# Performance work log

Measured on AMD Instinct MI355X. Metric: run time of the kernel, lower is better.

## Reference

```python
import jax, jax.numpy as jnp
import numpy as np

B, N, D = 64, 256, 768
ITER_STEPS = 1


def _linear_w(key, out_d, in_d):
    s = 1.0 / np.sqrt(in_d)
    return jax.random.uniform(key, (out_d, in_d), jnp.float32, -s, s)


def setup_inputs() -> dict:
    key = jax.random.key(0)
    ks = jax.random.split(key, 16)
    node = jax.random.normal(ks[0], (B, N, D), jnp.float32)
    node_mask = jnp.ones((B, N), jnp.int32)
    argument_graph = jax.random.randint(ks[1], (B, N, N), 0, 2, jnp.int32)
    punctuation_graph = jax.random.randint(ks[2], (B, N, N), 0, 2, jnp.int32)
    inp = {
        "node": node,
        "node_mask": node_mask,
        "argument_graph": argument_graph,
        "punctuation_graph": punctuation_graph,
        # node-relatedness scorer: Linear(D, 1, bias=True)
        "Wq": _linear_w(ks[3], 1, D),
        "bq": jnp.zeros((1,), jnp.float32),
        # self node fc: Linear(D, D, bias=True)
        "Ws": _linear_w(ks[4], D, D),
        "bs": jnp.zeros((D,), jnp.float32),
        # 8 relation projections, Linear(D, D, bias=False)
        "Wa": _linear_w(ks[5], D, D),
        "Wp": _linear_w(ks[6], D, D),
        "Wap": _linear_w(ks[7], D, D),
        "Wpp": _linear_w(ks[8], D, D),
        "Wa2": _linear_w(ks[9], D, D),
        "Wp2": _linear_w(ks[10], D, D),
        "Wap2": _linear_w(ks[11], D, D),
        "Wpp2": _linear_w(ks[12], D, D),
    }
    return inp


def reference(node, node_mask, argument_graph, punctuation_graph,
              Wq, bq, Ws, bs, Wa, Wp, Wap, Wpp, Wa2, Wp2, Wap2, Wpp2):
    f32 = jnp.float32
    mask = node_mask.astype(f32)                      # [B, N]
    n = node.shape[1]
    eye = jnp.eye(n, dtype=f32)
    # dd_graph: node_mask outer product with zeroed diagonal
    dd = mask[:, None, :] * mask[:, :, None] * (1.0 - eye)   # [B, N, N]
    g_a = dd * argument_graph.astype(f32)
    g_p = dd * punctuation_graph.astype(f32)
    # reverse directed edges
    g_ar = dd * jnp.swapaxes(g_a, 1, 2)
    g_pr = dd * jnp.swapaxes(g_p, 1, 2)
    neigh = g_a.sum(-1) + g_p.sum(-1) + g_ar.sum(-1) + g_pr.sum(-1)  # [B, N]
    denom = jnp.where(neigh >= 1.0, neigh, 1.0)

    all_weight = []
    for _ in range(ITER_STEPS):
        # (1) node relatedness
        dw = jax.nn.sigmoid(jnp.einsum('bnd,od->bno', node, Wq) + bq)[..., 0]  # [B, N]
        all_weight.append(dw)
        self_info = jnp.einsum('bnd,ed->bne', node, Ws) + bs

        def msg(g, W):
            # node_weight: broadcast dw over rows, zero where no edge
            nw = dw[:, None, :] * g                    # [B, N, N]
            proj = jnp.einsum('bnd,ed->bne', node, W)  # [B, N, D]
            return jnp.matmul(nw, proj)                # [B, N, D]

        agg = (msg(g_a, Wa) + msg(g_p, Wp) + msg(g_ar, Wap) + msg(g_pr, Wpp)
               + msg(g_a, Wa2) + msg(g_p, Wp2) + msg(g_ar, Wap2) + msg(g_pr, Wpp2))
        agg = agg / denom[..., None]
        # (3) node update
        node = jax.nn.relu(self_info + agg)

    all_weight = jnp.stack(all_weight, axis=1)  # [B, steps, N]
    return node, all_weight
```

## Files before the change

### kernel.cpp

```cpp
#include <hip/hip_runtime.h>
#include <hip/hip_bf16.h>
#include <math.h>

typedef __bf16 bf16;
typedef unsigned char u8;
typedef unsigned long long ull;
typedef __bf16 bf16x8 __attribute__((ext_vector_type(8)));
typedef float f32x4 __attribute__((ext_vector_type(4)));

#define BB 64
#define NN 256
#define DD 768
#define MM (BB*NN)
#define KP 1024
#define WSZ (DD*DD)
#define TL2 272
#define AROW2 196608


__device__ __forceinline__ void async16(const void* g, void* l) {
  __builtin_amdgcn_global_load_lds((__attribute__((address_space(1))) void*)g,
                                   (__attribute__((address_space(3))) void*)l,
                                   16, 0, 0);
}

__device__ __forceinline__ void mma_step_fp8t(const char* lA, const char* lB,
                                              f32x4 acc[4][4], int lane, int wr, int wc) {
  long af[4], bfr[4];
  int koq = (lane >> 4) * 1024;
  int mA = (wr * 64 + (lane & 15)) * 8;
  int mB = (wc * 64 + (lane & 15)) * 8;
#pragma unroll
  for (int r = 0; r < 4; ++r)
    af[r] = *(const long*)(lA + koq + mA + r * 128);
#pragma unroll
  for (int c = 0; c < 4; ++c)
    bfr[c] = *(const long*)(lB + koq + mB + c * 128);
#pragma unroll
  for (int r = 0; r < 4; ++r)
#pragma unroll
    for (int c = 0; c < 4; ++c)
      acc[r][c] = __builtin_amdgcn_mfma_f32_16x16x32_fp8_fp8(af[r], bfr[c], acc[r][c], 0, 0, 0);
}

__device__ __forceinline__ void mma_step_sw(const char* lA, const char* lB,
                                            f32x4 acc[4][4], int lane, int wr, int wc) {
  bf16x8 af[4], bfr[4];
  int rbase = wr * 64 + (lane & 15);
  int cbase = wc * 64 + (lane & 15);
  int sSw = ((lane >> 4) ^ (((lane & 15) >> 1) & 3)) * 16;
#pragma unroll
  for (int r = 0; r < 4; ++r)
    af[r] = *(const bf16x8*)(lA + (rbase + r * 16) * 64 + sSw);
#pragma unroll
  for (int c = 0; c < 4; ++c)
    bfr[c] = *(const bf16x8*)(lB + (cbase + c * 16) * 64 + sSw);
#pragma unroll
  for (int r = 0; r < 4; ++r)
#pragma unroll
    for (int c = 0; c < 4; ++c)
      acc[r][c] = __builtin_amdgcn_mfma_f32_16x16x32_bf16(af[r], bfr[c], acc[r][c], 0, 0, 0);
}

__device__ __forceinline__ unsigned pack4(float a, float b, float c, float d) {
  int w = 0;
  w = __builtin_amdgcn_cvt_pk_fp8_f32(a, b, w, false);
  w = __builtin_amdgcn_cvt_pk_fp8_f32(c, d, w, true);
  return (unsigned)w;
}

__global__ void k_pre(const float* __restrict__ node, const float* __restrict__ Wq,
                      const float* __restrict__ bq, bf16* __restrict__ node_bf,
                      float* __restrict__ dw, float* __restrict__ allw,
                      float* __restrict__ neigh,
                      const float* __restrict__ Ws,
                      const float* __restrict__ Wa, const float* __restrict__ Wp,
                      const float* __restrict__ Wap, const float* __restrict__ Wpp,
                      const float* __restrict__ Wa2, const float* __restrict__ Wp2,
                      const float* __restrict__ Wap2, const float* __restrict__ Wpp2,
                      bf16* __restrict__ Wcat4, bf16* __restrict__ Ws_bf) {
  if (blockIdx.x < MM / 4) {
    int lane = threadIdx.x & 63, wv = threadIdx.x >> 6;
    int row = blockIdx.x * 4 + wv;
    const float* nr = node + (size_t)row * DD;
    bf16* nb = node_bf + (size_t)row * DD;
    float s = 0.f;
#pragma unroll
    for (int k = 0; k < DD / 64; ++k) {
      int idx = lane + k * 64;
      float v = nr[idx];
      nb[idx] = (bf16)v;
      s += v * Wq[idx];
    }
#pragma unroll
    for (int off = 32; off; off >>= 1) s += __shfl_down(s, off);
    if (lane == 0) {
      float z = s + bq[0];
      float d = 1.f / (1.f + expf(-z));
      dw[row] = d;
      allw[row] = d;
      neigh[row] = 0.f;
    }
  } else {
    int i = (blockIdx.x - MM / 4) * 256 + threadIdx.x;
    Ws_bf[i] = (bf16)Ws[i];
    Wcat4[i]           = (bf16)(Wa[i] + Wa2[i]);
    Wcat4[i + WSZ]     = (bf16)(Wp[i] + Wp2[i]);
    Wcat4[i + 2 * WSZ] = (bf16)(Wap[i] + Wap2[i]);
    Wcat4[i + 3 * WSZ] = (bf16)(Wpp[i] + Wpp2[i]);
  }
}

__device__ __forceinline__ void store_tiled(u8* base, int tile, int kin, int m, uint4 v) {
  size_t o = (size_t)tile * 4096 + (size_t)((kin >> 3) * 1024 + m * 8);
  *(ull*)(base + o)        = ((ull)v.y << 32) | v.x;
  *(ull*)(base + o + 1024) = ((ull)v.w << 32) | v.z;
}

__global__ void k_graph(const int* __restrict__ mask, const int* __restrict__ arg,
                        const int* __restrict__ pun, const float* __restrict__ dw,
                        u8* __restrict__ g8, float* __restrict__ neigh) {
  __shared__ float la[64][65];
  __shared__ float lp[64][65];
  __shared__ float msk[256];
  __shared__ float dwv[256];
  int tid = threadIdx.x;
  int bi = blockIdx.x;
  int b = bi >> 4, it = (bi >> 2) & 3, jt = bi & 3;
  int i0 = it * 64, j0 = jt * 64;
  msk[tid] = (float)mask[b * NN + tid];
  dwv[tid] = dw[b * NN + tid];
  __syncthreads();
  int ir = tid >> 2, c4 = (tid & 3) * 16;
  int i = i0 + ir;
  float mi = msk[i];
  size_t gb = (size_t)b * NN * NN;
  const int* ap = arg + gb + (size_t)i * NN + j0 + c4;
  const int* pp = pun + gb + (size_t)i * NN + j0 + c4;
  float va[16], vp[16];
  float racc = 0.f;
#pragma unroll
  for (int k = 0; k < 16; ++k) {
    int j = j0 + c4 + k;
    float dd = (i == j) ? 0.f : mi * msk[j];
    float ga = dd * (float)ap[k];
    float gp = dd * (float)pp[k];
    la[ir][c4 + k] = ga;
    lp[ir][c4 + k] = gp;
    float w = dwv[j];
    va[k] = w * ga;
    vp[k] = w * gp;
    racc += ga + gp;
  }
  uint4 oa, op;
#pragma unroll
  for (int g = 0; g < 4; ++g) {
    (&oa.x)[g] = pack4(va[g*4], va[g*4+1], va[g*4+2], va[g*4+3]);
    (&op.x)[g] = pack4(vp[g*4], vp[g*4+1], vp[g*4+2], vp[g*4+3]);
  }
  {
    int tR = (b * 2 + (i >> 7)) * 32;
    int K0 = j0 + c4;
    store_tiled(g8, tR + (K0 >> 5),       K0 & 31, i & 127, oa);
    store_tiled(g8, tR + 8 + (K0 >> 5),   K0 & 31, i & 127, op);
  }
  racc += __shfl_xor(racc, 1);
  racc += __shfl_xor(racc, 2);
  if ((tid & 3) == 0) atomicAdd(&neigh[b * NN + i], racc);
  __syncthreads();
  int jr = ir, ic4 = c4;
  float cacc = 0.f;
#pragma unroll
  for (int k = 0; k < 16; ++k) {
    float ga = la[ic4 + k][jr];
    float gp = lp[ic4 + k][jr];
    float w = dwv[i0 + ic4 + k];
    va[k] = w * ga;
    vp[k] = w * gp;
    cacc += ga + gp;
  }
#pragma unroll
  for (int g = 0; g < 4; ++g) {
    (&oa.x)[g] = pack4(va[g*4], va[g*4+1], va[g*4+2], va[g*4+3]);
    (&op.x)[g] = pack4(vp[g*4], vp[g*4+1], vp[g*4+2], vp[g*4+3]);
  }
  {
    int row = j0 + jr;
    int tR = (b * 2 + (row >> 7)) * 32;
    int K2 = i0 + ic4;
    store_tiled(g8, tR + 16 + (K2 >> 5),  K2 & 31, row & 127, oa);
    store_tiled(g8, tR + 24 + (K2 >> 5),  K2 & 31, row & 127, op);
  }
  cacc += __shfl_xor(cacc, 1);
  cacc += __shfl_xor(cacc, 2);
  if ((tid & 3) == 0) atomicAdd(&neigh[b * NN + j0 + jr], cacc);
}

template<int T>
__device__ __forceinline__ void proj_ph(char* smem, int wvoff,
                                        const char* gA, const char* gB,
                                        int aoff, int boff,
                                        f32x4 (&acc)[8][4]) {
  const char* L = smem + (T & 3) * 32768;
  bf16x8 af[8], bfr[4];
#pragma unroll
  for (int r = 0; r < 8; ++r) af[r] = *(const bf16x8*)(L + aoff + r * 1024);
#pragma unroll
  for (int c = 0; c < 4; ++c) bfr[c] = *(const bf16x8*)(L + boff + c * 1024);
  if constexpr (T + 3 < 24) {
    char* D = smem + ((T + 3) & 3) * 32768 + wvoff;
    const char* sA = gA + (T + 3) * 64;
    const char* sB = gB + (T + 3) * 64;
    async16(sA,         D);
    async16(sA + AROW2, D + 8192);
    async16(sB,         D + 16384);
    async16(sB + AROW2, D + 24576);
  }
  __builtin_amdgcn_sched_barrier(0);
  __builtin_amdgcn_s_barrier();
  asm volatile("s_waitcnt lgkmcnt(0)" ::: "memory");
  __builtin_amdgcn_sched_barrier(0);
  __builtin_amdgcn_s_setprio(1);
#pragma unroll
  for (int r = 0; r < 8; ++r)
#pragma unroll
    for (int c = 0; c < 4; ++c)
      acc[r][c] = __builtin_amdgcn_mfma_f32_16x16x32_bf16(af[r], bfr[c], acc[r][c], 0, 0, 0);
  __builtin_amdgcn_s_setprio(0);
  if constexpr (T <= 20)      asm volatile("s_waitcnt vmcnt(8)" ::: "memory");
  else if constexpr (T == 21) asm volatile("s_waitcnt vmcnt(4)" ::: "memory");
  else if constexpr (T == 22) asm volatile("s_waitcnt vmcnt(0)" ::: "memory");
  __builtin_amdgcn_sched_barrier(0);
  __builtin_amdgcn_s_barrier();
}

__global__ __launch_bounds__(512, 2) void k_proj(const bf16* __restrict__ node_bf,
                                                 const bf16* __restrict__ Wcat4,
                                                 u8* __restrict__ p8) {
  __shared__ __align__(16) char smem[131072];
  int tid = threadIdx.x, lane = tid & 63, wv = tid >> 6;
  int wr = wv >> 2, wc = wv & 3;
  int l = blockIdx.x, xcd = l & 7, idx = l >> 3;
  int b = (idx / 12) * 8 + xcd;
  int nt = idx % 12;
  int n0 = nt * 256;
  int m0 = b * 256;
  int srcS = (tid & 3) ^ ((tid >> 3) & 3);
  const char* gA = (const char*)node_bf + (size_t)m0 * 1536 + (tid >> 2) * 1536 + srcS * 16;
  const char* gB = (const char*)Wcat4  + (size_t)n0 * 1536 + (tid >> 2) * 1536 + srcS * 16;
  int wvoff = wv * 1024;
  int sSwR = ((lane >> 4) ^ (((lane & 15) >> 1) & 3)) << 4;
  int aoff = (wr * 128 + (lane & 15)) * 64 + sSwR;
  int boff = 16384 + (wc * 64 + (lane & 15)) * 64 + sSwR;
  f32x4 z = {0.f, 0.f, 0.f, 0.f};
  f32x4 acc[8][4];
#pragma unroll
  for (int r = 0; r < 8; ++r)
#pragma unroll
    for (int c = 0; c < 4; ++c) acc[r][c] = z;
#pragma unroll
  for (int u = 0; u < 3; ++u) {
    char* D = smem + u * 32768 + wvoff;
    const char* sA = gA + u * 64;
    const char* sB = gB + u * 64;
    async16(sA,         D);
    async16(sA + AROW2, D + 8192);
    async16(sB,         D + 16384);
    async16(sB + AROW2, D + 24576);
  }
  asm volatile("s_waitcnt vmcnt(8)" ::: "memory");
  __builtin_amdgcn_s_barrier();
  __builtin_amdgcn_sched_barrier(0);
  proj_ph< 0>(smem, wvoff, gA, gB, aoff, boff, acc);
  proj_ph< 1>(smem, wvoff, gA, gB, aoff, boff, acc);
  proj_ph< 2>(smem, wvoff, gA, gB, aoff, boff, acc);
  proj_ph< 3>(smem, wvoff, gA, gB, aoff, boff, acc);
  proj_ph< 4>(smem, wvoff, gA, gB, aoff, boff, acc);
  proj_ph< 5>(smem, wvoff, gA, gB, aoff, boff, acc);
  proj_ph< 6>(smem, wvoff, gA, gB, aoff, boff, acc);
  proj_ph< 7>(smem, wvoff, gA, gB, aoff, boff, acc);
  proj_ph< 8>(smem, wvoff, gA, gB, aoff, boff, acc);
  proj_ph< 9>(smem, wvoff, gA, gB, aoff, boff, acc);
  proj_ph<10>(smem, wvoff, gA, gB, aoff, boff, acc);
  proj_ph<11>(smem, wvoff, gA, gB, aoff, boff, acc);
  proj_ph<12>(smem, wvoff, gA, gB, aoff, boff, acc);
  proj_ph<13>(smem, wvoff, gA, gB, aoff, boff, acc);
  proj_ph<14>(smem, wvoff, gA, gB, aoff, boff, acc);
  proj_ph<15>(smem, wvoff, gA, gB, aoff, boff, acc);
  proj_ph<16>(smem, wvoff, gA, gB, aoff, boff, acc);
  proj_ph<17>(smem, wvoff, gA, gB, aoff, boff, acc);
  proj_ph<18>(smem, wvoff, gA, gB, aoff, boff, acc);
  proj_ph<19>(smem, wvoff, gA, gB, aoff, boff, acc);
  proj_ph<20>(smem, wvoff, gA, gB, aoff, boff, acc);
  proj_ph<21>(smem, wvoff, gA, gB, aoff, boff, acc);
  proj_ph<22>(smem, wvoff, gA, gB, aoff, boff, acc);
  proj_ph<23>(smem, wvoff, gA, gB, aoff, boff, acc);
  __syncthreads();
  u8* tb = (u8*)smem;
  int X = n0 / DD, e0 = n0 % DD;
#pragma unroll
  for (int r = 0; r < 8; ++r)
#pragma unroll
    for (int c = 0; c < 4; ++c) {
      int n = wc * 64 + c * 16 + (lane & 15);
      int m = wr * 128 + r * 16 + ((lane >> 4) << 2);
      *(unsigned*)(tb + n * TL2 + m) =
          pack4(acc[r][c][0], acc[r][c][1], acc[r][c][2], acc[r][c][3]);
    }
  __syncthreads();
#pragma unroll
  for (int t2 = 0; t2 < 8; ++t2) {
    int erow = t2 * 32 + (tid & 31);
    int col = (tid >> 5) * 16;
    uint4 v = *(const uint4*)(tb + erow * TL2 + col);
    int e = e0 + erow;
    int tR = (b * 6 + (e >> 7)) * 32 + X * 8;
    store_tiled(p8, tR + (col >> 5), col & 31, e & 127, v);
  }
}

__global__ __launch_bounds__(256, 3) void k_agg(const u8* __restrict__ g8,
                                                const u8* __restrict__ p8,
                                                const bf16* __restrict__ node_bf,
                                                const bf16* __restrict__ Ws_bf,
                                                const float* __restrict__ neigh,
                                                const float* __restrict__ bs,
                                                float* __restrict__ out) {
  __shared__ __align__(16) char smem[49152];
  int tid = threadIdx.x, lane = tid & 63, wv = tid >> 6, wr = wv >> 1, wc = wv & 1;
  int l = blockIdx.x;
  int xcd = l & 7, idx = l >> 3;
  int b = (idx / 12) * 8 + xcd;
  int t = idx % 12;
  int i0 = (t / 6) * 128, e0 = (t % 6) * 128;
  f32x4 z = {0.f, 0.f, 0.f, 0.f};
  f32x4 acc[4][4];
#pragma unroll
  for (int r = 0; r < 4; ++r)
#pragma unroll
    for (int c = 0; c < 4; ++c) acc[r][c] = z;
  const u8* At = g8 + (size_t)((b * 2 + (i0 >> 7)) * 32) * 4096;
  const u8* Bt = p8 + (size_t)((b * 6 + (e0 >> 7)) * 32) * 4096;
  int gOff = tid * 16;
  int lOff = wv * 1024;
#pragma unroll
  for (int u = 0; u < 2; ++u) {
    char* D = smem + u * 16384 + lOff;
    const u8* a0 = At + (size_t)(2 * u) * 4096 + gOff;
    const u8* b0 = Bt + (size_t)(2 * u) * 4096 + gOff;
    async16(a0, D);            async16(a0 + 4096, D + 4096);
    async16(b0, D + 8192);     async16(b0 + 4096, D + 12288);
  }
  for (int s = 0; s < 16; ++s) {
    if (s <= 14) asm volatile("s_waitcnt vmcnt(4)" ::: "memory");
    else         asm volatile("s_waitcnt vmcnt(0)" ::: "memory");
    __builtin_amdgcn_s_barrier();
    if (s + 2 < 16) {
      char* D = smem + ((s + 2) % 3) * 16384 + lOff;
      const u8* a0 = At + (size_t)(2 * (s + 2)) * 4096 + gOff;
      const u8* b0 = Bt + (size_t)(2 * (s + 2)) * 4096 + gOff;
      async16(a0, D);          async16(a0 + 4096, D + 4096);
      async16(b0, D + 8192);   async16(b0 + 4096, D + 12288);
    }
    const char* L = smem + (s % 3) * 16384;
    __builtin_amdgcn_s_setprio(1);
    mma_step_fp8t(L,        L + 8192,  acc, lane, wr, wc);
    mma_step_fp8t(L + 4096, L + 12288, acc, lane, wr, wc);
    __builtin_amdgcn_s_setprio(0);
  }
  int rowb = i0 + wr * 64 + (lane >> 4) * 4;
#pragma unroll
  for (int r = 0; r < 4; ++r)
#pragma unroll
    for (int q = 0; q < 4; ++q) {
      float rd = 1.f / fmaxf(neigh[b * NN + rowb + r * 16 + q], 1.f);
#pragma unroll
      for (int c = 0; c < 4; ++c) acc[r][c][q] *= rd;
    }
  __syncthreads();
  const bf16* Ab2 = node_bf + (size_t)(b * NN + i0) * DD;
  const bf16* Bb2 = Ws_bf + (size_t)e0 * DD;
  int scol = ((lane & 3) ^ ((lane >> 3) & 3)) * 8;
#define STAGE2(u)                                                              \
  {                                                                            \
    char* D = smem + ((u) % 3) * 16384;                                        \
    _Pragma("unroll")                                                          \
    for (int cc = 0; cc < 2; ++cc) {                                           \
      int c = wv * 2 + cc;                                                     \
      int row = c * 16 + (lane >> 2);                                          \
      async16(Ab2 + (size_t)row * DD + (u) * 32 + scol, D + c * 1024);         \
      async16(Bb2 + (size_t)row * DD + (u) * 32 + scol, D + 8192 + c * 1024);  \
    }                                                                          \
  }
  STAGE2(0);
  STAGE2(1);
  for (int s = 0; s < 24; ++s) {
    if (s <= 22) asm volatile("s_waitcnt vmcnt(4)" ::: "memory");
    else         asm volatile("s_waitcnt vmcnt(0)" ::: "memory");
    __builtin_amdgcn_s_barrier();
    if (s + 2 < 24) STAGE2(s + 2);
    const char* L = smem + (s % 3) * 16384;
    __builtin_amdgcn_s_setprio(1);
    mma_step_sw(L, L + 8192, acc, lane, wr, wc);
    __builtin_amdgcn_s_setprio(0);
  }
#undef STAGE2
  int colb = e0 + wc * 64 + (lane & 15);
#pragma unroll
  for (int c = 0; c < 4; ++c) {
    int col = colb + c * 16;
    float bv = bs[col];
#pragma unroll
    for (int r = 0; r < 4; ++r)
#pragma unroll
      for (int q = 0; q < 4; ++q) {
        int m = b * NN + rowb + r * 16 + q;
        out[(size_t)m * DD + col] = fmaxf(acc[r][c][q] + bv, 0.f);
      }
  }
}

extern "C" void kernel_launch(void* const* d_in, const int* in_sizes, int n_in,
                              void* d_out, int out_size, void* d_ws, size_t ws_size,
                              hipStream_t stream) {
  const float* node = (const float*)d_in[0];
  const int* mask   = (const int*)d_in[1];
  const int* arg    = (const int*)d_in[2];
  const int* pun    = (const int*)d_in[3];
  const float* Wq   = (const float*)d_in[4];
  const float* bq   = (const float*)d_in[5];
  const float* Ws   = (const float*)d_in[6];
  const float* bs   = (const float*)d_in[7];
  const float* Wa   = (const float*)d_in[8];
  const float* Wp   = (const float*)d_in[9];
  const float* Wap  = (const float*)d_in[10];
  const float* Wpp  = (const float*)d_in[11];
  const float* Wa2  = (const float*)d_in[12];
  const float* Wp2  = (const float*)d_in[13];
  const float* Wap2 = (const float*)d_in[14];
  const float* Wpp2 = (const float*)d_in[15];

  float* out  = (float*)d_out;
  float* allw = out + (size_t)MM * DD;

  char* ws = (char*)d_ws;
  bf16* node_bf = (bf16*)ws;
  float* dw     = (float*)(ws + 25165824);
  float* neigh  = (float*)(ws + 25231360);
  bf16* Wcat4   = (bf16*)(ws + 25296896);
  bf16* Ws_bf   = (bf16*)(ws + 30015488);
  u8*   g8      = (u8*)(ws + 31195136);
  u8*   p8      = (u8*)(ws + 47972352);
  (void)ws_size; (void)in_sizes; (void)n_in; (void)out_size;

  k_pre<<<MM / 4 + WSZ / 256, 256, 0, stream>>>(node, Wq, bq, node_bf, dw, allw,
                                                neigh, Ws, Wa, Wp, Wap, Wpp,
                                                Wa2, Wp2, Wap2, Wpp2, Wcat4, Ws_bf);
  k_graph<<<BB * 16, 256, 0, stream>>>(mask, arg, pun, dw, g8, neigh);
  k_proj<<<768, 512, 0, stream>>>(node_bf, Wcat4, p8);
  k_agg<<<12 * BB, 256, 0, stream>>>(g8, p8, node_bf, Ws_bf, neigh, bs, out);
}
```

Before: 303.6 us.

## Shrink k_proj tile to 256x128 with 3-stage pipeline and higher occupancy

The projection GEMM tile is halved from 256x256 to 256x128 outputs per block, doubling the grid to 1536 blocks. The LDS pipeline drops from 4 stages of 32 KB to 3 stages of 24 KB, prefetching two steps ahead with redistributed per-wave async loads. This lets four blocks share a CU instead of two. The aim is better latency hiding and load balance, at the cost of re-reading the node tiles twice as often and a shallower prefetch.

```diff
diff --git a/kernel.cpp b/kernel.cpp
--- a/kernel.cpp
+++ b/kernel.cpp
@@ -15,7 +15,6 @@
 #define KP 1024
 #define WSZ (DD*DD)
 #define TL2 272
-#define AROW2 196608
 
 
 __device__ __forceinline__ void async16(const void* g, void* l) {
@@ -197,24 +196,20 @@
 }
 
 template<int T>
-__device__ __forceinline__ void proj_ph(char* smem, int wvoff,
-                                        const char* gA, const char* gB,
-                                        int aoff, int boff,
-                                        f32x4 (&acc)[8][4]) {
-  const char* L = smem + (T & 3) * 32768;
-  bf16x8 af[8], bfr[4];
-#pragma unroll
-  for (int r = 0; r < 8; ++r) af[r] = *(const bf16x8*)(L + aoff + r * 1024);
-#pragma unroll
-  for (int c = 0; c < 4; ++c) bfr[c] = *(const bf16x8*)(L + boff + c * 1024);
-  if constexpr (T + 3 < 24) {
-    char* D = smem + ((T + 3) & 3) * 32768 + wvoff;
-    const char* sA = gA + (T + 3) * 64;
-    const char* sB = gB + (T + 3) * 64;
-    async16(sA,         D);
-    async16(sA + AROW2, D + 8192);
-    async16(sB,         D + 16384);
-    async16(sB + AROW2, D + 24576);
+__device__ __forceinline__ void proj_ph(char* smem,
+                                        const char* const (&sb)[3], const int (&lo)[3],
+                                        int aoff, int boff, f32x4 (&acc)[4][4]) {
+  const char* L = smem + (T % 3) * 24576;
+  bf16x8 af[4], bfr[4];
+#pragma unroll
+  for (int r = 0; r < 4; ++r) af[r] = *(const bf16x8*)(L + aoff + r * 1024);
+#pragma unroll
+  for (int c = 0; c < 4; ++c) bfr[c] = *(const bf16x8*)(L + 16384 + boff + c * 1024);
+  if constexpr (T + 2 < 24) {
+    char* D = smem + ((T + 2) % 3) * 24576;
+#pragma unroll
+    for (int i = 0; i < 3; ++i)
+      async16(sb[i] + (T + 2) * 64, D + lo[i]);
   }
   __builtin_amdgcn_sched_barrier(0);
   __builtin_amdgcn_s_barrier();
@@ -222,100 +217,106 @@
   __builtin_amdgcn_sched_barrier(0);
   __builtin_amdgcn_s_setprio(1);
 #pragma unroll
-  for (int r = 0; r < 8; ++r)
+  for (int r = 0; r < 4; ++r)
 #pragma unroll
     for (int c = 0; c < 4; ++c)
       acc[r][c] = __builtin_amdgcn_mfma_f32_16x16x32_bf16(af[r], bfr[c], acc[r][c], 0, 0, 0);
   __builtin_amdgcn_s_setprio(0);
-  if constexpr (T <= 20)      asm volatile("s_waitcnt vmcnt(8)" ::: "memory");
-  else if constexpr (T == 21) asm volatile("s_waitcnt vmcnt(4)" ::: "memory");
+  if constexpr (T <= 21)      asm volatile("s_waitcnt vmcnt(3)" ::: "memory");
   else if constexpr (T == 22) asm volatile("s_waitcnt vmcnt(0)" ::: "memory");
   __builtin_amdgcn_sched_barrier(0);
   __builtin_amdgcn_s_barrier();
 }
 
-__global__ __launch_bounds__(512, 2) void k_proj(const bf16* __restrict__ node_bf,
+__global__ __launch_bounds__(512, 4) void k_proj(const bf16* __restrict__ node_bf,
                                                  const bf16* __restrict__ Wcat4,
                                                  u8* __restrict__ p8) {
-  __shared__ __align__(16) char smem[131072];
+  __shared__ __align__(16) char smem[73728];
   int tid = threadIdx.x, lane = tid & 63, wv = tid >> 6;
-  int wr = wv >> 2, wc = wv & 3;
+  int wr = wv >> 1, wc = wv & 1;
   int l = blockIdx.x, xcd = l & 7, idx = l >> 3;
-  int b = (idx / 12) * 8 + xcd;
-  int nt = idx % 12;
-  int n0 = nt * 256;
+  int b = (idx / 24) * 8 + xcd;
+  int nt = idx % 24;
+  int n0 = nt * 128;
   int m0 = b * 256;
   int srcS = (tid & 3) ^ ((tid >> 3) & 3);
-  const char* gA = (const char*)node_bf + (size_t)m0 * 1536 + (tid >> 2) * 1536 + srcS * 16;
-  const char* gB = (const char*)Wcat4  + (size_t)n0 * 1536 + (tid >> 2) * 1536 + srcS * 16;
-  int wvoff = wv * 1024;
+  const char* gAr = (const char*)node_bf + (size_t)m0 * 1536;
+  const char* gBr = (const char*)Wcat4  + (size_t)n0 * 1536;
+  const char* sb[3]; int lo[3];
+#pragma unroll
+  for (int i = 0; i < 3; ++i) {
+    int c = wv * 3 + i;
+    if (c < 16) {
+      sb[i] = gAr + (size_t)(c * 16 + (lane >> 2)) * 1536 + srcS * 16;
+      lo[i] = c * 1024;
+    } else {
+      sb[i] = gBr + (size_t)((c - 16) * 16 + (lane >> 2)) * 1536 + srcS * 16;
+      lo[i] = 16384 + (c - 16) * 1024;
+    }
+  }
   int sSwR = ((lane >> 4) ^ (((lane & 15) >> 1) & 3)) << 4;
-  int aoff = (wr * 128 + (lane & 15)) * 64 + sSwR;
-  int boff = 16384 + (wc * 64 + (lane & 15)) * 64 + sSwR;
+  int aoff = (wr * 64 + (lane & 15)) * 64 + sSwR;
+  int boff = (wc * 64 + (lane & 15)) * 64 + sSwR;
   f32x4 z = {0.f, 0.f, 0.f, 0.f};
-  f32x4 acc[8][4];
-#pragma unroll
-  for (int r = 0; r < 8; ++r)
+  f32x4 acc[4][4];
+#pragma unroll
+  for (int r = 0; r < 4; ++r)
 #pragma unroll
     for (int c = 0; c < 4; ++c) acc[r][c] = z;
 #pragma unroll
-  for (int u = 0; u < 3; ++u) {
-    char* D = smem + u * 32768 + wvoff;
-    const char* sA = gA + u * 64;
-    const char* sB = gB + u * 64;
-    async16(sA,         D);
-    async16(sA + AROW2, D + 8192);
-    async16(sB,         D + 16384);
-    async16(sB + AROW2, D + 24576);
-  }
-  asm volatile("s_waitcnt vmcnt(8)" ::: "memory");
+  for (int u = 0; u < 2; ++u) {
+    char* D = smem + u * 24576;
+#pragma unroll
+    for (int i = 0; i < 3; ++i)
+      async16(sb[i] + u * 64, D + lo[i]);
+  }
+  asm volatile("s_waitcnt vmcnt(3)" ::: "memory");
   __builtin_amdgcn_s_barrier();
   __builtin_amdgcn_sched_barrier(0);
-  proj_ph< 0>(smem, wvoff, gA, gB, aoff, boff, acc);
-  proj_ph< 1>(smem, wvoff, gA, gB, aoff, boff, acc);
-  proj_ph< 2>(smem, wvoff, gA, gB, aoff, boff, acc);
-  proj_ph< 3>(smem, wvoff, gA, gB, aoff, boff, acc);
-  proj_ph< 4>(smem, wvoff, gA, gB, aoff, boff, acc);
-  proj_ph< 5>(smem, wvoff, gA, gB, aoff, boff, acc);
-  proj_ph< 6>(smem, wvoff, gA, gB, aoff, boff, acc);
-  proj_ph< 7>(smem, wvoff, gA, gB, aoff, boff, acc);
-  proj_ph< 8>(smem, wvoff, gA, gB, aoff, boff, acc);
-  proj_ph< 9>(smem, wvoff, gA, gB, aoff, boff, acc);
-  proj_ph<10>(smem, wvoff, gA, gB, aoff, boff, acc);
-  proj_ph<11>(smem, wvoff, gA, gB, aoff, boff, acc);
-  proj_ph<12>(smem, wvoff, gA, gB, aoff, boff, acc);
-  proj_ph<13>(smem, wvoff, gA, gB, aoff, boff, acc);
-  proj_ph<14>(smem, wvoff, gA, gB, aoff, boff, acc);
-  proj_ph<15>(smem, wvoff, gA, gB, aoff, boff, acc);
-  proj_ph<16>(smem, wvoff, gA, gB, aoff, boff, acc);
-  proj_ph<17>(smem, wvoff, gA, gB, aoff, boff, acc);
-  proj_ph<18>(smem, wvoff, gA, gB, aoff, boff, acc);
-  proj_ph<19>(smem, wvoff, gA, gB, aoff, boff, acc);
-  proj_ph<20>(smem, wvoff, gA, gB, aoff, boff, acc);
-  proj_ph<21>(smem, wvoff, gA, gB, aoff, boff, acc);
-  proj_ph<22>(smem, wvoff, gA, gB, aoff, boff, acc);
-  proj_ph<23>(smem, wvoff, gA, gB, aoff, boff, acc);
+  proj_ph< 0>(smem, sb, lo, aoff, boff, acc);
+  proj_ph< 1>(smem, sb, lo, aoff, boff, acc);
+  proj_ph< 2>(smem, sb, lo, aoff, boff, acc);
+  proj_ph< 3>(smem, sb, lo, aoff, boff, acc);
+  proj_ph< 4>(smem, sb, lo, aoff, boff, acc);
+  proj_ph< 5>(smem, sb, lo, aoff, boff, acc);
+  proj_ph< 6>(smem, sb, lo, aoff, boff, acc);
+  proj_ph< 7>(smem, sb, lo, aoff, boff, acc);
+  proj_ph< 8>(smem, sb, lo, aoff, boff, acc);
+  proj_ph< 9>(smem, sb, lo, aoff, boff, acc);
+  proj_ph<10>(smem, sb, lo, aoff, boff, acc);
+  proj_ph<11>(smem, sb, lo, aoff, boff, acc);
+  proj_ph<12>(smem, sb, lo, aoff, boff, acc);
+  proj_ph<13>(smem, sb, lo, aoff, boff, acc);
+  proj_ph<14>(smem, sb, lo, aoff, boff, acc);
+  proj_ph<15>(smem, sb, lo, aoff, boff, acc);
+  proj_ph<16>(smem, sb, lo, aoff, boff, acc);
+  proj_ph<17>(smem, sb, lo, aoff, boff, acc);
+  proj_ph<18>(smem, sb, lo, aoff, boff, acc);
+  proj_ph<19>(smem, sb, lo, aoff, boff, acc);
+  proj_ph<20>(smem, sb, lo, aoff, boff, acc);
+  proj_ph<21>(smem, sb, lo, aoff, boff, acc);
+  proj_ph<22>(smem, sb, lo, aoff, boff, acc);
+  proj_ph<23>(smem, sb, lo, aoff, boff, acc);
   __syncthreads();
   u8* tb = (u8*)smem;
   int X = n0 / DD, e0 = n0 % DD;
 #pragma unroll
-  for (int r = 0; r < 8; ++r)
+  for (int r = 0; r < 4; ++r)
 #pragma unroll
     for (int c = 0; c < 4; ++c) {
       int n = wc * 64 + c * 16 + (lane & 15);
-      int m = wr * 128 + r * 16 + ((lane >> 4) << 2);
+      int m = wr * 64 + r * 16 + ((lane >> 4) << 2);
       *(unsigned*)(tb + n * TL2 + m) =
           pack4(acc[r][c][0], acc[r][c][1], acc[r][c][2], acc[r][c][3]);
     }
   __syncthreads();
-#pragma unroll
-  for (int t2 = 0; t2 < 8; ++t2) {
-    int erow = t2 * 32 + (tid & 31);
-    int col = (tid >> 5) * 16;
-    uint4 v = *(const uint4*)(tb + erow * TL2 + col);
-    int e = e0 + erow;
-    int tR = (b * 6 + (e >> 7)) * 32 + X * 8;
-    store_tiled(p8, tR + (col >> 5), col & 31, e & 127, v);
+  int tR = (b * 6 + (e0 >> 7)) * 32 + X * 8;
+#pragma unroll
+  for (int t2 = 0; t2 < 4; ++t2) {
+    int row = t2 * 32 + (tid >> 4);
+    int col = (tid & 15) * 16;
+    uint4 v = *(const uint4*)(tb + row * TL2 + col);
+    store_tiled(p8, tR + (col >> 5), col & 31, row, v);
   }
 }
 
@@ -457,6 +458,6 @@
                                                 neigh, Ws, Wa, Wp, Wap, Wpp,
                                                 Wa2, Wp2, Wap2, Wpp2, Wcat4, Ws_bf);
   k_graph<<<BB * 16, 256, 0, stream>>>(mask, arg, pun, dw, g8, neigh);
-  k_proj<<<768, 512, 0, stream>>>(node_bf, Wcat4, p8);
+  k_proj<<<1536, 512, 0, stream>>>(node_bf, Wcat4, p8);
   k_agg<<<12 * BB, 256, 0, stream>>>(g8, p8, node_bf, Ws_bf, neigh, bs, out);
 }
```

New measurement: 309.9 us. 1.02x slower.
